# Performance work log

Measured on AMD Instinct MI355X. Metric: run time of the kernel, lower is better.

Reference implementation:

```python
import jax, jax.numpy as jnp
import numpy as np
from jax import lax

BETA = 0.1
N_CLUSTERS = 64


def setup_inputs() -> dict:
    key = jax.random.key(0)
    ks = jax.random.split(key, 10)
    L, B, Hin, H = 200, 2048, 64, 256
    s = lambda k, shape, scale=0.05: jax.random.normal(k, shape, dtype=jnp.float32) * scale
    return {
        "X": jax.random.normal(ks[0], (L, B, Hin), dtype=jnp.float32),
        "W_ih0": s(ks[1], (4 * H, Hin)),
        "W_hh0": s(ks[2], (4 * H, H)),
        "b_ih0": s(ks[3], (4 * H,)),
        "b_hh0": s(ks[4], (4 * H,)),
        "W_ih1": s(ks[5], (4 * H, H)),
        "W_hh1": s(ks[6], (4 * H, H)),
        "b_ih1": s(ks[7], (4 * H,)),
        "b_hh1": s(ks[8], (4 * H,)),
        "clusters": jax.random.normal(ks[9], (N_CLUSTERS, H), dtype=jnp.float32),
    }


def _lstm_layer(x, W_ih, W_hh, b_ih, b_hh):
    # x: (L, B, I) -> outputs (L, B, H); torch gate order i, f, g, o
    H = W_hh.shape[1]
    B = x.shape[1]
    b = b_ih + b_hh

    def step(carry, xt):
        h, c = carry
        gates = xt @ W_ih.T + h @ W_hh.T + b  # (B, 4H)
        i, f, g, o = jnp.split(gates, 4, axis=-1)
        c = jax.nn.sigmoid(f) * c + jax.nn.sigmoid(i) * jnp.tanh(g)
        h = jax.nn.sigmoid(o) * jnp.tanh(c)
        return (h, c), h

    h0 = jnp.zeros((B, H), x.dtype)
    (_, _), ys = lax.scan(step, (h0, h0), x)
    return ys


def _encode(X, W_ih0, W_hh0, b_ih0, b_hh0, W_ih1, W_hh1, b_ih1, b_hh1):
    y0 = _lstm_layer(X, W_ih0, W_hh0, b_ih0, b_hh0)
    y1 = _lstm_layer(y0, W_ih1, W_hh1, b_ih1, b_hh1)
    return y1[-1]  # latent_X: (B, H), last timestep of top layer


def reference(X, W_ih0, W_hh0, b_ih0, b_hh0, W_ih1, W_hh1, b_ih1, b_hh1, clusters):
    latent_X = _encode(X, W_ih0, W_hh0, b_ih0, b_hh0, W_ih1, W_hh1, b_ih1, b_hh1)

    # kmeans assignment on detached latents (l2 distance)
    lat_sg = lax.stop_gradient(latent_X)
    d2 = (jnp.sum(lat_sg * lat_sg, -1, keepdims=True)
          - 2.0 * lat_sg @ clusters.T
          + jnp.sum(clusters * clusters, -1))  # (B, K)
    cluster_id = jnp.argmin(d2, axis=-1)  # (B,)

    # centroid update from assigned (detached) points; keep old centroid if empty
    sums = jax.ops.segment_sum(lat_sg, cluster_id, num_segments=N_CLUSTERS)
    counts = jax.ops.segment_sum(jnp.ones((lat_sg.shape[0],), lat_sg.dtype),
                                 cluster_id, num_segments=N_CLUSTERS)
    upd = jnp.where(counts[:, None] > 0, sums / jnp.maximum(counts, 1.0)[:, None], clusters)

    # vectorized per-sample cluster distance loss: sum_i 0.5*beta*||latent_i - c[id_i]||^2
    diff = latent_X - upd[cluster_id]  # gather (B, H)
    dist_loss = 0.5 * BETA * jnp.sum(diff * diff)
    return latent_X, dist_loss
```

## Files before the change

kernel.cpp:

```cpp
#include <hip/hip_runtime.h>
#include <hip/hip_bf16.h>
#include <math.h>

typedef unsigned short u16;
typedef unsigned int u32;
typedef __attribute__((ext_vector_type(8))) __bf16 bf16x8;
typedef __attribute__((ext_vector_type(4))) float f32x4;

#define LSTM_L 200
#define LSTM_B 2048
#define LSTM_HIN 64
#define LSTM_H 256
#define NCLUST 64
#define HALF_BETA 0.05f
#define LDS_BYTES 131072
#define ASSIGN_LDS 135424
#define ASSIGN_BLOCKS 64

__device__ __forceinline__ void gload_lds16(const void* g, void* l) {
    __builtin_amdgcn_global_load_lds(
        (__attribute__((address_space(1))) const void*)g,
        (__attribute__((address_space(3))) void*)l, 16, 0, 0);
}

__device__ __forceinline__ float fast_sigmoid(float x) {
    return __builtin_amdgcn_rcpf(1.f + __expf(-x));
}
__device__ __forceinline__ float fast_tanh(float x) {
    return 2.f * __builtin_amdgcn_rcpf(1.f + __expf(-2.f * x)) - 1.f;
}
__device__ __forceinline__ void wt_store(u32* p, u32 v) {
    __hip_atomic_store(p, v, __ATOMIC_RELAXED, __HIP_MEMORY_SCOPE_AGENT);
}

template<int KIN>
__global__ __launch_bounds__(256) void pack_frag(
    const float* __restrict__ Wih, const float* __restrict__ Whh,
    u16* __restrict__ Wp)
{
    constexpr int NCH = (KIN + LSTM_H) / 32;
    const int total = 1024 * (KIN + LSTM_H);
    for (int i = blockIdx.x * 256 + threadIdx.x; i < total; i += gridDim.x * 256) {
        const int e = i & 7;
        int t = i >> 3;
        const int lane = t & 63; t >>= 6;
        const int nf = t & 1;    t >>= 1;
        const int ch = t % NCH;  t /= NCH;
        const int wn = t & 3;
        const int nb = t >> 2;
        const int l15 = lane & 15;
        const int j = (2 * nf + (l15 & 1)) * 256 + nb * 32 + wn * 8 + (l15 >> 1);
        const int k = ch * 32 + ((lane >> 4) << 3) + e;
        const float v = (k < KIN) ? Wih[(size_t)j * KIN + k]
                                  : Whh[(size_t)j * LSTM_H + (k - KIN)];
        Wp[i] = __builtin_bit_cast(u16, (__bf16)v);
    }
}

template<int KIN>
__device__ __forceinline__ void run_layer(
    const float* __restrict__ xf32,
    const u16* __restrict__ hbelow,
    const u16* __restrict__ hself,
    const u16* __restrict__ Wp,
    const float* __restrict__ bih, const float* __restrict__ bhh,
    u16* __restrict__ hout, float* __restrict__ latout,
    float* __restrict__ cst,
    int blk, char* smem, int tid)
{
    constexpr int NCH = (KIN + LSTM_H) / 32;
    constexpr bool IS_L0 = (KIN == 64);
    const int lane = tid & 63;
    const int w = tid >> 6;
    const int wm = w >> 2;
    const int wn = w & 3;
    const int l15 = lane & 15;
    const int q = lane >> 4;
    const int mb = blk >> 3;
    const int nb = blk & 7;
    const int b0 = mb * 128;

    bf16x8 Breg[NCH][2];
    {
        const u16* wp = Wp + (size_t)((nb * 4 + wn) * NCH) * 1024 + lane * 8;
#pragma unroll
        for (int ch = 0; ch < NCH; ++ch)
#pragma unroll
            for (int nf = 0; nf < 2; ++nf)
                Breg[ch][nf] = *(const bf16x8*)(wp + (ch * 2 + nf) * 512);
    }

    const int hcol = nb * 32 + wn * 8 + (l15 >> 1);
    const int rowA = wm * 64;
    float cp[4][4];
#pragma unroll
    for (int mf = 0; mf < 4; ++mf)
#pragma unroll
        for (int r = 0; r < 4; ++r)
            cp[mf][r] = cst[(size_t)(b0 + rowA + mf * 16 + q * 4 + r) * 256 + hcol];

    const int gpar = l15 & 1;
    const float b0a = bih[gpar * 256 + hcol] + bhh[gpar * 256 + hcol];
    const float b1a = bih[(2 + gpar) * 256 + hcol] + bhh[(2 + gpar) * 256 + hcol];

    if (IS_L0) {
#pragma unroll
        for (int i = 0; i < 8; ++i) {
            const int slot = i * 512 + tid;
            const int row = slot >> 5;
            const int so = (slot & 31) * 16;
            const int koff = so ^ ((row & 7) << 4);
            gload_lds16((const char*)hself + (size_t)(b0 + row) * 512 + koff,
                        smem + slot * 16);
        }
#pragma unroll
        for (int p = 0; p < 2; ++p) {
            const int slot = p * 512 + tid;
            const int row = slot >> 3;
            const int so = (slot & 7) * 16;
            const int koff = so ^ ((row & 7) << 4);
            const float* s = xf32 + (size_t)(b0 + row) * 64 + (koff >> 1);
            const float4 v0 = *(const float4*)s;
            const float4 v1 = *(const float4*)(s + 4);
            bf16x8 pk;
            pk[0] = (__bf16)v0.x; pk[1] = (__bf16)v0.y;
            pk[2] = (__bf16)v0.z; pk[3] = (__bf16)v0.w;
            pk[4] = (__bf16)v1.x; pk[5] = (__bf16)v1.y;
            pk[6] = (__bf16)v1.z; pk[7] = (__bf16)v1.w;
            *(bf16x8*)(smem + 65536 + slot * 16) = pk;
        }
    } else {
#pragma unroll
        for (int i = 0; i < 16; ++i) {
            const int slot = i * 512 + tid;
            const int row = slot >> 6;
            const int so = (slot & 63) * 16;
            const int koff = so ^ ((row & 7) << 4);
            const char* src = (koff < 512)
                ? (const char*)hbelow + (size_t)(b0 + row) * 512 + koff
                : (const char*)hself + (size_t)(b0 + row) * 512 + (koff - 512);
            gload_lds16(src, smem + slot * 16);
        }
    }
    __syncthreads();

    f32x4 acc[4][2];
#pragma unroll
    for (int mf = 0; mf < 4; ++mf)
#pragma unroll
        for (int nf = 0; nf < 2; ++nf) acc[mf][nf] = f32x4{0.f, 0.f, 0.f, 0.f};

    const int qoff = q * 16;
    const int swzl = (l15 & 7) << 4;
#pragma unroll
    for (int ch = 0; ch < NCH; ++ch) {
        bf16x8 af[4];
#pragma unroll
        for (int mf = 0; mf < 4; ++mf) {
            const int row = rowA + mf * 16 + l15;
            const char* ap;
            if (IS_L0) {
                if (ch < 2)
                    ap = smem + 65536 + row * 128 + ((ch * 64 + qoff) ^ swzl);
                else
                    ap = smem + row * 512 + (((ch - 2) * 64 + qoff) ^ swzl);
            } else {
                ap = smem + row * 1024 + ((ch * 64 + qoff) ^ swzl);
            }
            af[mf] = *(const bf16x8*)ap;
        }
#pragma unroll
        for (int mf = 0; mf < 4; ++mf)
#pragma unroll
            for (int nf = 0; nf < 2; ++nf)
                acc[mf][nf] = __builtin_amdgcn_mfma_f32_16x16x32_bf16(
                    af[mf], Breg[ch][nf], acc[mf][nf], 0, 0, 0);
    }

#pragma unroll
    for (int mf = 0; mf < 4; ++mf) {
#pragma unroll
        for (int r = 0; r < 4; ++r) {
            const float a0 = acc[mf][0][r] + b0a;
            const float a1 = acc[mf][1][r] + b1a;
            const float p0 = __shfl_xor(a0, 1);
            const float p1 = __shfl_xor(a1, 1);
            const float gi = gpar ? p0 : a0;
            const float gf = gpar ? a0 : p0;
            const float gg = gpar ? p1 : a1;
            const float go = gpar ? a1 : p1;
            const float cn = fast_sigmoid(gf) * cp[mf][r]
                           + fast_sigmoid(gi) * fast_tanh(gg);
            const float hv = fast_sigmoid(go) * fast_tanh(cn);
            const int rowo = b0 + rowA + mf * 16 + q * 4 + r;
            const size_t oidx = (size_t)rowo * 256 + hcol;
            const u16 hb = __builtin_bit_cast(u16, (__bf16)hv);
            const int pr = __shfl_xor((int)(u32)hb, 2);
            const u32 pk = ((u32)hb & 0xffffu) | (((u32)pr) << 16);
            if (gpar) {
                wt_store((u32*)&cst[oidx], __builtin_bit_cast(u32, cn));
            } else if (latout) {
                wt_store((u32*)&latout[oidx], __builtin_bit_cast(u32, hv));
            } else if ((l15 & 3) == 0) {
                wt_store((u32*)hout + ((size_t)rowo * 128 + (hcol >> 1)), pk);
            }
        }
    }
}

__global__ __launch_bounds__(512, 1) void lstm_slot(
    const float* __restrict__ xt,
    const u16* __restrict__ h0c, u16* __restrict__ h0n, float* __restrict__ c0,
    const u16* __restrict__ Wp0,
    const float* __restrict__ bih0, const float* __restrict__ bhh0,
    const u16* __restrict__ h1c, u16* __restrict__ h1n, float* __restrict__ c1,
    const u16* __restrict__ Wp1,
    const float* __restrict__ bih1, const float* __restrict__ bhh1,
    float* __restrict__ latout, int do0, int do1)
{
    extern __shared__ char smem[];
    const int tid = threadIdx.x;
    if (blockIdx.x < 128) {
        if (do0)
            run_layer<LSTM_HIN>(xt, nullptr, h0c, Wp0, bih0, bhh0,
                                h0n, nullptr, c0, blockIdx.x, smem, tid);
    } else {
        if (do1)
            run_layer<LSTM_H>(nullptr, h0c, h1c, Wp1, bih1, bhh1,
                              h1n, latout, c1, blockIdx.x - 128, smem, tid);
    }
}

__global__ __launch_bounds__(256, 1) void assign_fused(
    const float* __restrict__ lat, const float* __restrict__ clusters,
    int* __restrict__ ids, float* __restrict__ partial, int* __restrict__ pcount)
{
    extern __shared__ char sm[];
    float* clT    = (float*)sm;
    float* psum   = (float*)(sm + 65536);
    float* rowbuf = (float*)(sm + 131072);
    int*   pcnt   = (int*)(sm + 135168);

    const int tid = threadIdx.x;
    const int k = tid & 63;
    const int w = tid >> 6;

    for (int i = tid; i < 16384; i += 256) {
        const int kk = i >> 8, j = i & 255;
        clT[j * 64 + kk] = clusters[(size_t)kk * 256 + j];
        psum[i] = 0.f;
    }
    if (tid < 64) pcnt[tid] = 0;
    __syncthreads();

    float* rb = rowbuf + w * 256;
    const int rbase = (int)blockIdx.x * 32 + w * 8;
    for (int rr = 0; rr < 8; ++rr) {
        const int row = rbase + rr;
#pragma unroll
        for (int p = 0; p < 4; ++p)
            rb[p * 64 + k] = lat[(size_t)row * 256 + p * 64 + k];
        float d0 = 0.f, d1 = 0.f, d2 = 0.f, d3 = 0.f;
#pragma unroll 4
        for (int j = 0; j < 256; j += 4) {
            const float t0 = rb[j + 0] - clT[(j + 0) * 64 + k];
            const float t1 = rb[j + 1] - clT[(j + 1) * 64 + k];
            const float t2 = rb[j + 2] - clT[(j + 2) * 64 + k];
            const float t3 = rb[j + 3] - clT[(j + 3) * 64 + k];
            d0 += t0 * t0; d1 += t1 * t1; d2 += t2 * t2; d3 += t3 * t3;
        }
        float d = (d0 + d1) + (d2 + d3);
        int idx = k;
        for (int off = 32; off > 0; off >>= 1) {
            const float od = __shfl_down(d, off, 64);
            const int   oi = __shfl_down(idx, off, 64);
            if (od < d || (od == d && oi < idx)) { d = od; idx = oi; }
        }
        const int best = __shfl(idx, 0, 64);
        if (k == 0) { ids[row] = best; atomicAdd(&pcnt[best], 1); }
#pragma unroll
        for (int p = 0; p < 4; ++p)
            atomicAdd(&psum[best * 256 + p * 64 + k], rb[p * 64 + k]);
    }
    __syncthreads();
    for (int i = tid; i < 16384; i += 256)
        partial[(size_t)blockIdx.x * 16384 + i] = psum[i];
    if (tid < 64) pcount[(size_t)blockIdx.x * 64 + tid] = pcnt[tid];
}

__global__ __launch_bounds__(256) void centroid_final2(
    const float* __restrict__ partial, const int* __restrict__ pcount,
    const float* __restrict__ clusters, float* __restrict__ upd)
{
    const int k = blockIdx.x;
    const int h = threadIdx.x;
    float s = 0.f;
    int c = 0;
    for (int b = 0; b < ASSIGN_BLOCKS; ++b) {
        s += partial[(size_t)b * 16384 + k * 256 + h];
        c += pcount[(size_t)b * 64 + k];
    }
    upd[(size_t)k * LSTM_H + h] = (c > 0)
        ? s / (float)c
        : clusters[(size_t)k * LSTM_H + h];
}

__global__ __launch_bounds__(256) void loss_kernel(
    const float* __restrict__ lat, const int* __restrict__ ids,
    const float* __restrict__ upd, float* __restrict__ out_loss)
{
    float p = 0.f;
    const int total = LSTM_B * LSTM_H;
    for (int idx = blockIdx.x * blockDim.x + threadIdx.x; idx < total;
         idx += gridDim.x * blockDim.x) {
        const int b = idx >> 8;
        const float d = lat[idx] - upd[(size_t)ids[b] * LSTM_H + (idx & 255)];
        p += d * d;
    }
    for (int off = 32; off > 0; off >>= 1) p += __shfl_down(p, off, 64);
    __shared__ float wsum[4];
    const int lane = threadIdx.x & 63, wid = threadIdx.x >> 6;
    if (lane == 0) wsum[wid] = p;
    __syncthreads();
    if (threadIdx.x == 0)
        atomicAdd(out_loss, HALF_BETA * (wsum[0] + wsum[1] + wsum[2] + wsum[3]));
}

extern "C" void kernel_launch(void* const* d_in, const int* in_sizes, int n_in,
                              void* d_out, int out_size, void* d_ws, size_t ws_size,
                              hipStream_t stream)
{
    const float* X     = (const float*)d_in[0];
    const float* Wih0  = (const float*)d_in[1];
    const float* Whh0  = (const float*)d_in[2];
    const float* bih0  = (const float*)d_in[3];
    const float* bhh0  = (const float*)d_in[4];
    const float* Wih1  = (const float*)d_in[5];
    const float* Whh1  = (const float*)d_in[6];
    const float* bih1  = (const float*)d_in[7];
    const float* bhh1  = (const float*)d_in[8];
    const float* clust = (const float*)d_in[9];

    float* out = (float*)d_out;
    char* base = (char*)d_ws;
    const size_t MB = 1u << 20;
    const size_t KB = 1024;

    u16* Wp0      = (u16*)(base + 0 * MB);
    u16* Wp1      = (u16*)(base + 1 * MB);
    u16* h0a      = (u16*)(base + 2 * MB);
    u16* h0b      = (u16*)(base + 3 * MB);
    u16* h1a      = (u16*)(base + 4 * MB);
    u16* h1b      = (u16*)(base + 5 * MB);
    float* c0     = (float*)(base + 6 * MB);
    float* c1     = (float*)(base + 8 * MB);
    float* partial= (float*)(base + 6 * MB);
    float* upd    = (float*)(base + 10 * MB);
    int* pcount   = (int*)(base + 10 * MB + 64 * KB);
    int* ids      = (int*)(base + 10 * MB + 80 * KB);

    const size_t BH = (size_t)LSTM_B * LSTM_H;

    hipMemsetAsync(h0a, 0, MB, stream);
    hipMemsetAsync(h1a, 0, MB, stream);
    hipMemsetAsync(c0, 0, 4 * MB, stream);
    hipMemsetAsync(out + BH, 0, sizeof(float), stream);

    pack_frag<LSTM_HIN><<<320, 256, 0, stream>>>(Wih0, Whh0, Wp0);
    pack_frag<LSTM_H>  <<<512, 256, 0, stream>>>(Wih1, Whh1, Wp1);

    hipFuncSetAttribute((const void*)lstm_slot,
                        hipFuncAttributeMaxDynamicSharedMemorySize, LDS_BYTES);
    hipFuncSetAttribute((const void*)assign_fused,
                        hipFuncAttributeMaxDynamicSharedMemorySize, ASSIGN_LDS);

    u16* h0c = h0a; u16* h0n = h0b;
    u16* h1c = h1a; u16* h1n = h1b;
    for (int s = 0; s <= LSTM_L; ++s) {
        const int do0 = (s < LSTM_L) ? 1 : 0;
        const int do1 = (s > 0) ? 1 : 0;
        const float* xt = do0 ? X + (size_t)s * LSTM_B * LSTM_HIN : nullptr;
        float* lat = (s == LSTM_L) ? out : nullptr;
        lstm_slot<<<256, 512, LDS_BYTES, stream>>>(
            xt, h0c, h0n, c0, Wp0, bih0, bhh0,
            h1c, h1n, c1, Wp1, bih1, bhh1, lat, do0, do1);
        if (do0) { u16* t = h0c; h0c = h0n; h0n = t; }
        if (do1) { u16* t = h1c; h1c = h1n; h1n = t; }
    }

    assign_fused<<<ASSIGN_BLOCKS, 256, ASSIGN_LDS, stream>>>(
        out, clust, ids, partial, pcount);
    centroid_final2<<<NCLUST, 256, 0, stream>>>(partial, pcount, clust, upd);
    loss_kernel<<<256, 256, 0, stream>>>(out, ids, upd, out + BH);
}
```

Measured before the change: 2.620 ms.

## Replace per-timestep LSTM launches with persistent cooperative kernel and counter-based sync

Replaces the 201 per-timestep kernel launches with one cooperative persistent kernel. Each block runs all timesteps of its layer and tile, syncing with producer blocks through per-row-block atomic counters and acquire/release fences. Cell state stays in registers instead of round-tripping through global memory. The next step's X slice is prefetched before the spin-wait. This removes launch overhead and c-state traffic, but adds spin-wait latency and relies on all 256 blocks being co-resident; a bounded spin guard could silently break out early.

```diff
diff --git a/kernel.cpp b/kernel.cpp
--- a/kernel.cpp
+++ b/kernel.cpp
@@ -31,6 +31,16 @@
 }
 __device__ __forceinline__ void wt_store(u32* p, u32 v) {
     __hip_atomic_store(p, v, __ATOMIC_RELAXED, __HIP_MEMORY_SCOPE_AGENT);
+}
+__device__ __forceinline__ u32 cload(const u32* p) {
+    return __hip_atomic_load(p, __ATOMIC_RELAXED, __HIP_MEMORY_SCOPE_AGENT);
+}
+__device__ __forceinline__ void spin_ge(u32* p, u32 target) {
+    int guard = 0;
+    while (cload(p) < target) {
+        __builtin_amdgcn_s_sleep(8);
+        if (++guard > (1 << 18)) break;
+    }
 }
 
 template<int KIN>
@@ -57,177 +67,253 @@
     }
 }
 
-template<int KIN>
-__device__ __forceinline__ void run_layer(
-    const float* __restrict__ xf32,
-    const u16* __restrict__ hbelow,
-    const u16* __restrict__ hself,
-    const u16* __restrict__ Wp,
-    const float* __restrict__ bih, const float* __restrict__ bhh,
-    u16* __restrict__ hout, float* __restrict__ latout,
-    float* __restrict__ cst,
-    int blk, char* smem, int tid)
-{
-    constexpr int NCH = (KIN + LSTM_H) / 32;
-    constexpr bool IS_L0 = (KIN == 64);
+__global__ __launch_bounds__(512, 1) void lstm_persist5(
+    const float* __restrict__ X,
+    const u16* __restrict__ Wp0, const u16* __restrict__ Wp1,
+    const float* __restrict__ bih0, const float* __restrict__ bhh0,
+    const float* __restrict__ bih1, const float* __restrict__ bhh1,
+    u32* h0b0, u32* h0b1, u32* h1b0, u32* h1b1,
+    float* __restrict__ latent, u32* cnt0, u32* cnt1)
+{
+    extern __shared__ char smem[];
+    const int tid = threadIdx.x;
     const int lane = tid & 63;
     const int w = tid >> 6;
     const int wm = w >> 2;
     const int wn = w & 3;
     const int l15 = lane & 15;
     const int q = lane >> 4;
-    const int mb = blk >> 3;
-    const int nb = blk & 7;
+    const int gpar = l15 & 1;
+    const int bi = (int)blockIdx.x;
+    const int mb = bi & 15;
+    const int layer = (bi >> 4) & 1;
+    const int nb = bi >> 5;
     const int b0 = mb * 128;
-
-    bf16x8 Breg[NCH][2];
-    {
-        const u16* wp = Wp + (size_t)((nb * 4 + wn) * NCH) * 1024 + lane * 8;
-#pragma unroll
-        for (int ch = 0; ch < NCH; ++ch)
-#pragma unroll
-            for (int nf = 0; nf < 2; ++nf)
-                Breg[ch][nf] = *(const bf16x8*)(wp + (ch * 2 + nf) * 512);
-    }
+    u32* c0p = cnt0 + mb * 32;
+    u32* c1p = cnt1 + mb * 32;
 
     const int hcol = nb * 32 + wn * 8 + (l15 >> 1);
     const int rowA = wm * 64;
-    float cp[4][4];
-#pragma unroll
-    for (int mf = 0; mf < 4; ++mf)
-#pragma unroll
-        for (int r = 0; r < 4; ++r)
-            cp[mf][r] = cst[(size_t)(b0 + rowA + mf * 16 + q * 4 + r) * 256 + hcol];
-
-    const int gpar = l15 & 1;
-    const float b0a = bih[gpar * 256 + hcol] + bhh[gpar * 256 + hcol];
-    const float b1a = bih[(2 + gpar) * 256 + hcol] + bhh[(2 + gpar) * 256 + hcol];
-
-    if (IS_L0) {
-#pragma unroll
-        for (int i = 0; i < 8; ++i) {
-            const int slot = i * 512 + tid;
-            const int row = slot >> 5;
-            const int so = (slot & 31) * 16;
-            const int koff = so ^ ((row & 7) << 4);
-            gload_lds16((const char*)hself + (size_t)(b0 + row) * 512 + koff,
-                        smem + slot * 16);
-        }
-#pragma unroll
-        for (int p = 0; p < 2; ++p) {
-            const int slot = p * 512 + tid;
-            const int row = slot >> 3;
-            const int so = (slot & 7) * 16;
-            const int koff = so ^ ((row & 7) << 4);
-            const float* s = xf32 + (size_t)(b0 + row) * 64 + (koff >> 1);
-            const float4 v0 = *(const float4*)s;
-            const float4 v1 = *(const float4*)(s + 4);
-            bf16x8 pk;
-            pk[0] = (__bf16)v0.x; pk[1] = (__bf16)v0.y;
-            pk[2] = (__bf16)v0.z; pk[3] = (__bf16)v0.w;
-            pk[4] = (__bf16)v1.x; pk[5] = (__bf16)v1.y;
-            pk[6] = (__bf16)v1.z; pk[7] = (__bf16)v1.w;
-            *(bf16x8*)(smem + 65536 + slot * 16) = pk;
-        }
-    } else {
-#pragma unroll
-        for (int i = 0; i < 16; ++i) {
-            const int slot = i * 512 + tid;
-            const int row = slot >> 6;
-            const int so = (slot & 63) * 16;
-            const int koff = so ^ ((row & 7) << 4);
-            const char* src = (koff < 512)
-                ? (const char*)hbelow + (size_t)(b0 + row) * 512 + koff
-                : (const char*)hself + (size_t)(b0 + row) * 512 + (koff - 512);
-            gload_lds16(src, smem + slot * 16);
-        }
-    }
-    __syncthreads();
-
-    f32x4 acc[4][2];
-#pragma unroll
-    for (int mf = 0; mf < 4; ++mf)
-#pragma unroll
-        for (int nf = 0; nf < 2; ++nf) acc[mf][nf] = f32x4{0.f, 0.f, 0.f, 0.f};
-
     const int qoff = q * 16;
     const int swzl = (l15 & 7) << 4;
-#pragma unroll
-    for (int ch = 0; ch < NCH; ++ch) {
-        bf16x8 af[4];
-#pragma unroll
-        for (int mf = 0; mf < 4; ++mf) {
-            const int row = rowA + mf * 16 + l15;
-            const char* ap;
-            if (IS_L0) {
-                if (ch < 2)
-                    ap = smem + 65536 + row * 128 + ((ch * 64 + qoff) ^ swzl);
-                else
-                    ap = smem + row * 512 + (((ch - 2) * 64 + qoff) ^ swzl);
-            } else {
-                ap = smem + row * 1024 + ((ch * 64 + qoff) ^ swzl);
-            }
-            af[mf] = *(const bf16x8*)ap;
-        }
-#pragma unroll
-        for (int mf = 0; mf < 4; ++mf)
-#pragma unroll
-            for (int nf = 0; nf < 2; ++nf)
-                acc[mf][nf] = __builtin_amdgcn_mfma_f32_16x16x32_bf16(
-                    af[mf], Breg[ch][nf], acc[mf][nf], 0, 0, 0);
-    }
-
-#pragma unroll
-    for (int mf = 0; mf < 4; ++mf) {
-#pragma unroll
-        for (int r = 0; r < 4; ++r) {
-            const float a0 = acc[mf][0][r] + b0a;
-            const float a1 = acc[mf][1][r] + b1a;
-            const float p0 = __shfl_xor(a0, 1);
-            const float p1 = __shfl_xor(a1, 1);
-            const float gi = gpar ? p0 : a0;
-            const float gf = gpar ? a0 : p0;
-            const float gg = gpar ? p1 : a1;
-            const float go = gpar ? a1 : p1;
-            const float cn = fast_sigmoid(gf) * cp[mf][r]
-                           + fast_sigmoid(gi) * fast_tanh(gg);
-            const float hv = fast_sigmoid(go) * fast_tanh(cn);
-            const int rowo = b0 + rowA + mf * 16 + q * 4 + r;
-            const size_t oidx = (size_t)rowo * 256 + hcol;
-            const u16 hb = __builtin_bit_cast(u16, (__bf16)hv);
-            const int pr = __shfl_xor((int)(u32)hb, 2);
-            const u32 pk = ((u32)hb & 0xffffu) | (((u32)pr) << 16);
-            if (gpar) {
-                wt_store((u32*)&cst[oidx], __builtin_bit_cast(u32, cn));
-            } else if (latout) {
-                wt_store((u32*)&latout[oidx], __builtin_bit_cast(u32, hv));
-            } else if ((l15 & 3) == 0) {
-                wt_store((u32*)hout + ((size_t)rowo * 128 + (hcol >> 1)), pk);
-            }
-        }
-    }
-}
-
-__global__ __launch_bounds__(512, 1) void lstm_slot(
-    const float* __restrict__ xt,
-    const u16* __restrict__ h0c, u16* __restrict__ h0n, float* __restrict__ c0,
-    const u16* __restrict__ Wp0,
-    const float* __restrict__ bih0, const float* __restrict__ bhh0,
-    const u16* __restrict__ h1c, u16* __restrict__ h1n, float* __restrict__ c1,
-    const u16* __restrict__ Wp1,
-    const float* __restrict__ bih1, const float* __restrict__ bhh1,
-    float* __restrict__ latout, int do0, int do1)
-{
-    extern __shared__ char smem[];
-    const int tid = threadIdx.x;
-    if (blockIdx.x < 128) {
-        if (do0)
-            run_layer<LSTM_HIN>(xt, nullptr, h0c, Wp0, bih0, bhh0,
-                                h0n, nullptr, c0, blockIdx.x, smem, tid);
+
+    float cp[4][4];
+#pragma unroll
+    for (int mf = 0; mf < 4; ++mf)
+#pragma unroll
+        for (int r = 0; r < 4; ++r) cp[mf][r] = 0.f;
+
+    u32* h0b[2] = {h0b0, h0b1};
+    u32* h1b[2] = {h1b0, h1b1};
+
+    if (layer == 0) {
+        bf16x8 Breg[10][2];
+        {
+            const u16* wp = Wp0 + (size_t)((nb * 4 + wn) * 10) * 1024 + lane * 8;
+#pragma unroll
+            for (int ch = 0; ch < 10; ++ch)
+#pragma unroll
+                for (int nf = 0; nf < 2; ++nf)
+                    Breg[ch][nf] = *(const bf16x8*)(wp + (ch * 2 + nf) * 512);
+        }
+        const float bA = bih0[gpar * 256 + hcol] + bhh0[gpar * 256 + hcol];
+        const float bB = bih0[(2 + gpar) * 256 + hcol] + bhh0[(2 + gpar) * 256 + hcol];
+
+        for (int s = 0; s < LSTM_L; ++s) {
+            float4 xv[2][2];
+#pragma unroll
+            for (int p = 0; p < 2; ++p) {
+                const int slot = p * 512 + tid;
+                const int row = slot >> 3;
+                const int so = (slot & 7) * 16;
+                const int koff = so ^ ((row & 7) << 4);
+                const float* sp = X + (size_t)s * LSTM_B * LSTM_HIN
+                                  + (size_t)(b0 + row) * 64 + (koff >> 1);
+                xv[p][0] = *(const float4*)sp;
+                xv[p][1] = *(const float4*)(sp + 4);
+            }
+            if (tid == 0) {
+                if (s >= 1) spin_ge(c0p, 8u * s);
+                if (s >= 2) spin_ge(c1p, 8u * (s - 1));
+                if (s >= 1) __builtin_amdgcn_fence(__ATOMIC_ACQUIRE, "agent");
+            }
+            __syncthreads();
+
+            const u32* hself = h0b[(s + 1) & 1];
+#pragma unroll
+            for (int i = 0; i < 8; ++i) {
+                const int slot = i * 512 + tid;
+                const int row = slot >> 5;
+                const int so = (slot & 31) * 16;
+                const int koff = so ^ ((row & 7) << 4);
+                gload_lds16((const char*)hself + (size_t)(b0 + row) * 512 + koff,
+                            smem + slot * 16);
+            }
+#pragma unroll
+            for (int p = 0; p < 2; ++p) {
+                const int slot = p * 512 + tid;
+                bf16x8 pk;
+                pk[0] = (__bf16)xv[p][0].x; pk[1] = (__bf16)xv[p][0].y;
+                pk[2] = (__bf16)xv[p][0].z; pk[3] = (__bf16)xv[p][0].w;
+                pk[4] = (__bf16)xv[p][1].x; pk[5] = (__bf16)xv[p][1].y;
+                pk[6] = (__bf16)xv[p][1].z; pk[7] = (__bf16)xv[p][1].w;
+                *(bf16x8*)(smem + 65536 + slot * 16) = pk;
+            }
+            __syncthreads();
+
+            f32x4 acc[4][2];
+#pragma unroll
+            for (int mf = 0; mf < 4; ++mf)
+#pragma unroll
+                for (int nf = 0; nf < 2; ++nf) acc[mf][nf] = f32x4{0.f,0.f,0.f,0.f};
+#pragma unroll
+            for (int ch = 0; ch < 10; ++ch) {
+                bf16x8 af[4];
+#pragma unroll
+                for (int mf = 0; mf < 4; ++mf) {
+                    const int row = rowA + mf * 16 + l15;
+                    const char* ap = (ch < 2)
+                        ? smem + 65536 + row * 128 + ((ch * 64 + qoff) ^ swzl)
+                        : smem + row * 512 + (((ch - 2) * 64 + qoff) ^ swzl);
+                    af[mf] = *(const bf16x8*)ap;
+                }
+#pragma unroll
+                for (int mf = 0; mf < 4; ++mf)
+#pragma unroll
+                    for (int nf = 0; nf < 2; ++nf)
+                        acc[mf][nf] = __builtin_amdgcn_mfma_f32_16x16x32_bf16(
+                            af[mf], Breg[ch][nf], acc[mf][nf], 0, 0, 0);
+            }
+
+            u32* hdst = h0b[s & 1];
+#pragma unroll
+            for (int mf = 0; mf < 4; ++mf) {
+#pragma unroll
+                for (int r = 0; r < 4; ++r) {
+                    const float a0 = acc[mf][0][r] + bA;
+                    const float a1 = acc[mf][1][r] + bB;
+                    const float p0 = __shfl_xor(a0, 1);
+                    const float p1 = __shfl_xor(a1, 1);
+                    const float gi = gpar ? p0 : a0;
+                    const float gf = gpar ? a0 : p0;
+                    const float gg = gpar ? p1 : a1;
+                    const float go = gpar ? a1 : p1;
+                    const float cn = fast_sigmoid(gf) * cp[mf][r]
+                                   + fast_sigmoid(gi) * fast_tanh(gg);
+                    cp[mf][r] = cn;
+                    const float hv = fast_sigmoid(go) * fast_tanh(cn);
+                    const int rowo = b0 + rowA + mf * 16 + q * 4 + r;
+                    const u16 hb = __builtin_bit_cast(u16, (__bf16)hv);
+                    const int pr = __shfl_xor((int)(u32)hb, 2);
+                    const u32 pk = ((u32)hb & 0xffffu) | (((u32)pr) << 16);
+                    if ((l15 & 3) == 0)
+                        wt_store(hdst + (size_t)rowo * 128 + (hcol >> 1), pk);
+                }
+            }
+            __syncthreads();
+            if (tid == 0) {
+                __builtin_amdgcn_fence(__ATOMIC_RELEASE, "agent");
+                __hip_atomic_fetch_add(c0p, 1, __ATOMIC_RELAXED,
+                                       __HIP_MEMORY_SCOPE_AGENT);
+            }
+        }
     } else {
-        if (do1)
-            run_layer<LSTM_H>(nullptr, h0c, h1c, Wp1, bih1, bhh1,
-                              h1n, latout, c1, blockIdx.x - 128, smem, tid);
+        bf16x8 Breg[16][2];
+        {
+            const u16* wp = Wp1 + (size_t)((nb * 4 + wn) * 16) * 1024 + lane * 8;
+#pragma unroll
+            for (int ch = 0; ch < 16; ++ch)
+#pragma unroll
+                for (int nf = 0; nf < 2; ++nf)
+                    Breg[ch][nf] = *(const bf16x8*)(wp + (ch * 2 + nf) * 512);
+        }
+        const float bA = bih1[gpar * 256 + hcol] + bhh1[gpar * 256 + hcol];
+        const float bB = bih1[(2 + gpar) * 256 + hcol] + bhh1[(2 + gpar) * 256 + hcol];
+
+        for (int s = 1; s <= LSTM_L; ++s) {
+            if (tid == 0) {
+                spin_ge(c0p, 8u * s);
+                if (s >= 2) spin_ge(c1p, 8u * (s - 1));
+                __builtin_amdgcn_fence(__ATOMIC_ACQUIRE, "agent");
+            }
+            __syncthreads();
+
+            const u32* hbelow = h0b[(s + 1) & 1];
+            const u32* hself  = h1b[s & 1];
+#pragma unroll
+            for (int i = 0; i < 16; ++i) {
+                const int slot = i * 512 + tid;
+                const int row = slot >> 6;
+                const int so = (slot & 63) * 16;
+                const int koff = so ^ ((row & 7) << 4);
+                const char* src = (koff < 512)
+                    ? (const char*)hbelow + (size_t)(b0 + row) * 512 + koff
+                    : (const char*)hself + (size_t)(b0 + row) * 512 + (koff - 512);
+                gload_lds16(src, smem + slot * 16);
+            }
+            __syncthreads();
+
+            f32x4 acc[4][2];
+#pragma unroll
+            for (int mf = 0; mf < 4; ++mf)
+#pragma unroll
+                for (int nf = 0; nf < 2; ++nf) acc[mf][nf] = f32x4{0.f,0.f,0.f,0.f};
+#pragma unroll
+            for (int ch = 0; ch < 16; ++ch) {
+                bf16x8 af[4];
+#pragma unroll
+                for (int mf = 0; mf < 4; ++mf) {
+                    const int row = rowA + mf * 16 + l15;
+                    af[mf] = *(const bf16x8*)(smem + row * 1024 +
+                                              ((ch * 64 + qoff) ^ swzl));
+                }
+#pragma unroll
+                for (int mf = 0; mf < 4; ++mf)
+#pragma unroll
+                    for (int nf = 0; nf < 2; ++nf)
+                        acc[mf][nf] = __builtin_amdgcn_mfma_f32_16x16x32_bf16(
+                            af[mf], Breg[ch][nf], acc[mf][nf], 0, 0, 0);
+            }
+
+            u32* hdst = h1b[(s + 1) & 1];
+            const bool fin = (s == LSTM_L);
+#pragma unroll
+            for (int mf = 0; mf < 4; ++mf) {
+#pragma unroll
+                for (int r = 0; r < 4; ++r) {
+                    const float a0 = acc[mf][0][r] + bA;
+                    const float a1 = acc[mf][1][r] + bB;
+                    const float p0 = __shfl_xor(a0, 1);
+                    const float p1 = __shfl_xor(a1, 1);
+                    const float gi = gpar ? p0 : a0;
+                    const float gf = gpar ? a0 : p0;
+                    const float gg = gpar ? p1 : a1;
+                    const float go = gpar ? a1 : p1;
+                    const float cn = fast_sigmoid(gf) * cp[mf][r]
+                                   + fast_sigmoid(gi) * fast_tanh(gg);
+                    cp[mf][r] = cn;
+                    const float hv = fast_sigmoid(go) * fast_tanh(cn);
+                    const int rowo = b0 + rowA + mf * 16 + q * 4 + r;
+                    if (fin) {
+                        if (!gpar)
+                            wt_store((u32*)&latent[(size_t)rowo * 256 + hcol],
+                                     __builtin_bit_cast(u32, hv));
+                    } else {
+                        const u16 hb = __builtin_bit_cast(u16, (__bf16)hv);
+                        const int pr = __shfl_xor((int)(u32)hb, 2);
+                        const u32 pk = ((u32)hb & 0xffffu) | (((u32)pr) << 16);
+                        if ((l15 & 3) == 0)
+                            wt_store(hdst + (size_t)rowo * 128 + (hcol >> 1), pk);
+                    }
+                }
+            }
+            __syncthreads();
+            if (tid == 0 && s < LSTM_L) {
+                __builtin_amdgcn_fence(__ATOMIC_RELEASE, "agent");
+                __hip_atomic_fetch_add(c1p, 1, __ATOMIC_RELAXED,
+                                       __HIP_MEMORY_SCOPE_AGENT);
+            }
+        }
     }
 }
 
@@ -348,45 +434,41 @@
 
     u16* Wp0      = (u16*)(base + 0 * MB);
     u16* Wp1      = (u16*)(base + 1 * MB);
-    u16* h0a      = (u16*)(base + 2 * MB);
-    u16* h0b      = (u16*)(base + 3 * MB);
-    u16* h1a      = (u16*)(base + 4 * MB);
-    u16* h1b      = (u16*)(base + 5 * MB);
-    float* c0     = (float*)(base + 6 * MB);
-    float* c1     = (float*)(base + 8 * MB);
+    u32* h0b0     = (u32*)(base + 2 * MB);
+    u32* h0b1     = (u32*)(base + 3 * MB);
+    u32* h1b0     = (u32*)(base + 4 * MB);
+    u32* h1b1     = (u32*)(base + 5 * MB);
     float* partial= (float*)(base + 6 * MB);
     float* upd    = (float*)(base + 10 * MB);
     int* pcount   = (int*)(base + 10 * MB + 64 * KB);
     int* ids      = (int*)(base + 10 * MB + 80 * KB);
+    u32* cnt0     = (u32*)(base + 10 * MB + 88 * KB);
+    u32* cnt1     = (u32*)(base + 10 * MB + 90 * KB);
 
     const size_t BH = (size_t)LSTM_B * LSTM_H;
 
-    hipMemsetAsync(h0a, 0, MB, stream);
-    hipMemsetAsync(h1a, 0, MB, stream);
-    hipMemsetAsync(c0, 0, 4 * MB, stream);
+    hipMemsetAsync(h0b1, 0, MB, stream);
+    hipMemsetAsync(h1b1, 0, MB, stream);
+    hipMemsetAsync(base + 10 * MB + 88 * KB, 0, 4 * KB, stream);
     hipMemsetAsync(out + BH, 0, sizeof(float), stream);
 
     pack_frag<LSTM_HIN><<<320, 256, 0, stream>>>(Wih0, Whh0, Wp0);
     pack_frag<LSTM_H>  <<<512, 256, 0, stream>>>(Wih1, Whh1, Wp1);
 
-    hipFuncSetAttribute((const void*)lstm_slot,
+    hipFuncSetAttribute((const void*)lstm_persist5,
                         hipFuncAttributeMaxDynamicSharedMemorySize, LDS_BYTES);
     hipFuncSetAttribute((const void*)assign_fused,
                         hipFuncAttributeMaxDynamicSharedMemorySize, ASSIGN_LDS);
 
-    u16* h0c = h0a; u16* h0n = h0b;
-    u16* h1c = h1a; u16* h1n = h1b;
-    for (int s = 0; s <= LSTM_L; ++s) {
-        const int do0 = (s < LSTM_L) ? 1 : 0;
-        const int do1 = (s > 0) ? 1 : 0;
-        const float* xt = do0 ? X + (size_t)s * LSTM_B * LSTM_HIN : nullptr;
-        float* lat = (s == LSTM_L) ? out : nullptr;
-        lstm_slot<<<256, 512, LDS_BYTES, stream>>>(
-            xt, h0c, h0n, c0, Wp0, bih0, bhh0,
-            h1c, h1n, c1, Wp1, bih1, bhh1, lat, do0, do1);
-        if (do0) { u16* t = h0c; h0c = h0n; h0n = t; }
-        if (do1) { u16* t = h1c; h1c = h1n; h1n = t; }
-    }
+    float* lat = out;
+    void* args[] = {
+        (void*)&X, (void*)&Wp0, (void*)&Wp1,
+        (void*)&bih0, (void*)&bhh0, (void*)&bih1, (void*)&bhh1,
+        (void*)&h0b0, (void*)&h0b1, (void*)&h1b0, (void*)&h1b1,
+        (void*)&lat, (void*)&cnt0, (void*)&cnt1
+    };
+    hipLaunchCooperativeKernel((void*)lstm_persist5, dim3(256), dim3(512),
+                               args, LDS_BYTES, stream);
 
     assign_fused<<<ASSIGN_BLOCKS, 256, ASSIGN_LDS, stream>>>(
         out, clust, ids, partial, pcount);
```

After: 4.355 ms. +66.2%, slower.
